# Kernel tuning notes

Measured on AMD Instinct MI355X. Metric: run time of the kernel, lower is better.

The kernel has to match this reference:

```python
import jax, jax.numpy as jnp
import numpy as np

L, D, H, IMG, P, B, E = 12, 768, 12, 224, 16, 32, 512
HD = D // H            # 64
FF = 4 * D             # 3072
SEQ = (IMG // P) ** 2 + 1  # 197


def _ln(x, w, b, eps=1e-5):
    m = x.mean(-1, keepdims=True)
    v = jnp.mean((x - m) ** 2, axis=-1, keepdims=True)
    return (x - m) * jax.lax.rsqrt(v + eps) * w + b


def setup_inputs() -> dict:
    key = jax.random.key(0)
    ks = jax.random.split(key, 10)
    r = lambda k, shape, s=0.02: (jax.random.normal(k, shape, jnp.float32) * s)
    return {
        'image': jax.random.normal(ks[0], (B, 3, IMG, IMG), jnp.float32),
        'conv_w': r(ks[1], (D, 3, P, P)),
        'cls_emb': r(ks[2], (D,)),
        'pos_emb': r(ks[3], (SEQ, D)),
        'ln_pre_w': jnp.ones((D,), jnp.float32), 'ln_pre_b': jnp.zeros((D,), jnp.float32),
        'ln1_w': jnp.ones((L, D), jnp.float32), 'ln1_b': jnp.zeros((L, D), jnp.float32),
        'qkv_w': r(ks[4], (L, 3 * D, D)), 'qkv_b': jnp.zeros((L, 3 * D), jnp.float32),
        'out_w': r(ks[5], (L, D, D)), 'out_b': jnp.zeros((L, D), jnp.float32),
        'ln2_w': jnp.ones((L, D), jnp.float32), 'ln2_b': jnp.zeros((L, D), jnp.float32),
        'fc_w': r(ks[6], (L, FF, D)), 'fc_b': jnp.zeros((L, FF), jnp.float32),
        'pr_w': r(ks[7], (L, D, FF)), 'pr_b': jnp.zeros((L, D), jnp.float32),
        'ln_post_w': jnp.ones((D,), jnp.float32), 'ln_post_b': jnp.zeros((D,), jnp.float32),
        'proj': r(ks[8], (D, E)),
    }


def reference(image, conv_w, cls_emb, pos_emb, ln_pre_w, ln_pre_b,
              ln1_w, ln1_b, qkv_w, qkv_b, out_w, out_b,
              ln2_w, ln2_b, fc_w, fc_b, pr_w, pr_b,
              ln_post_w, ln_post_b, proj):
    # patchify: conv stride=kernel=patch, no bias -> [B, D, 14, 14]
    x = jax.lax.conv_general_dilated(image, conv_w, (P, P), 'VALID',
                                     dimension_numbers=('NCHW', 'OIHW', 'NCHW'))
    x = x.reshape(B, D, -1).transpose(0, 2, 1)               # [B, 196, D]
    cls = jnp.broadcast_to(cls_emb, (B, 1, D))
    x = jnp.concatenate([cls, x], axis=1) + pos_emb          # [B, SEQ, D]
    x = _ln(x, ln_pre_w, ln_pre_b)
    x = x.transpose(1, 0, 2)                                  # [SEQ, B, D]
    scale = 1.0 / np.sqrt(HD).astype(np.float32)

    def step(x, p):
        l1w, l1b, qw, qb, ow, ob, l2w, l2b, fw, fb, pw, pb = p
        h = _ln(x, l1w, l1b)
        qkv = h @ qw.T + qb                                    # [SEQ, B, 3D]
        q, k, v = jnp.split(qkv, 3, axis=-1)
        heads = lambda t: t.reshape(SEQ, B * H, HD).transpose(1, 0, 2)  # [B*H, SEQ, HD]
        q = heads(q) * scale
        k = heads(k)
        v = heads(v)
        a = jax.nn.softmax(jnp.einsum('nsh,nth->nst', q, k), axis=-1)   # [B*H, SEQ, SEQ]
        o = jnp.einsum('nst,nth->nsh', a, v)                  # [B*H, SEQ, HD]
        o = o.transpose(1, 0, 2).reshape(SEQ, B, D)
        x = x + (o @ ow.T + ob)
        h = _ln(x, l2w, l2b)
        h = jax.nn.gelu(h @ fw.T + fb, approximate=False)      # torch nn.GELU (exact)
        x = x + (h @ pw.T + pb)
        return x, None

    x, _ = jax.lax.scan(step, x, (ln1_w, ln1_b, qkv_w, qkv_b, out_w, out_b,
                                  ln2_w, ln2_b, fc_w, fc_b, pr_w, pr_b))
    x = x.transpose(1, 0, 2)                                   # [B, SEQ, D]
    cls_tok = _ln(x[:, 0, :], ln_post_w, ln_post_b)
    feats = cls_tok @ proj                                     # [B, E]
    return feats / jnp.linalg.norm(feats, axis=-1, keepdims=True)
```

## Files before the change

### kernel.cpp

```cpp
#include <hip/hip_runtime.h>
#include <stdint.h>

#define SEQ 197
#define NB 32
#define NH 12
#define NTOK (SEQ*NB)
#define MPAD 6400
#define NPATCH 6272

typedef unsigned short u16;
typedef unsigned int u32;
typedef __attribute__((ext_vector_type(8))) short bv8;
typedef __attribute__((ext_vector_type(4))) float f32x4;

__device__ __forceinline__ u16 f2bf(float f){
  u32 u = __float_as_uint(f);
  u = (u + 0x7fffu + ((u >> 16) & 1u)) >> 16;
  return (u16)u;
}
__device__ __forceinline__ float bf2f(u16 h){ return __uint_as_float(((u32)h) << 16); }

#if defined(__has_builtin)
#if __has_builtin(__builtin_amdgcn_global_load_lds)
#define HAS_GLLDS 1
#endif
#endif

__device__ __forceinline__ void gl_lds16(const void* g, void* l){
#ifdef HAS_GLLDS
  __builtin_amdgcn_global_load_lds(
      (const __attribute__((address_space(1))) void*)(uintptr_t)g,
      (__attribute__((address_space(3))) void*)(u32)(uintptr_t)l, 16, 0, 0);
#else
  int lane = threadIdx.x & 63;
  uint4 v = *(const uint4*)((const char*)g);
  *(uint4*)((char*)l + lane*16) = v;
#endif
}

__device__ __forceinline__ void red2(float& a, float& b){
  #pragma unroll
  for (int o = 32; o > 0; o >>= 1){ a += __shfl_down(a, o); b += __shfl_down(b, o); }
  __shared__ float red[8];
  int w = threadIdx.x >> 6, ln = threadIdx.x & 63;
  if (ln == 0){ red[w] = a; red[4 + w] = b; }
  __syncthreads();
  a = red[0] + red[1] + red[2] + red[3];
  b = red[4] + red[5] + red[6] + red[7];
}

__global__ __launch_bounds__(256) void cvt_k(const float* __restrict__ src, u16* __restrict__ dst, int n4){
  int i = blockIdx.x * 256 + threadIdx.x;
  if (i >= n4) return;
  float4 f = ((const float4*)src)[i];
  u32 lo = (u32)f2bf(f.x) | ((u32)f2bf(f.y) << 16);
  u32 hi = (u32)f2bf(f.z) | ((u32)f2bf(f.w) << 16);
  ((uint2*)dst)[i] = make_uint2(lo, hi);
}

__global__ __launch_bounds__(256) void im2col_k(const float* __restrict__ img, u16* __restrict__ Ap){
  int gid = blockIdx.x * 256 + threadIdx.x;
  int row = gid / 768, k = gid - row * 768;
  int b = row / 196, p = row - b * 196;
  int pr = p / 14, pc = p - pr * 14;
  int c = k >> 8, r = k & 255;
  int ph = r >> 4, pw = r & 15;
  size_t src = ((size_t)(b * 3 + c) * 224 + (pr * 16 + ph)) * 224 + (pc * 16 + pw);
  Ap[gid] = f2bf(img[src]);
}

template<int EPI>
__global__ __launch_bounds__(256, 2)
void gemm_sw(const u16* __restrict__ A, const u16* __restrict__ Bw,
             const float* __restrict__ bias, float* __restrict__ Cf,
             u16* __restrict__ Cb, int N, int K, int Mreal,
             int RM, int RN, int tmT, int tnT)
{
  __shared__ __align__(16) u16 sA[128 * 64];
  __shared__ __align__(16) u16 sB[128 * 64];
  const int xcd = blockIdx.x & 7, pos = blockIdx.x >> 3;
  const int xm = xcd >> 1, xn = xcd & 1;
  const int tm = xm * RM + pos / RN;
  const int tn = xn * RN + pos % RN;
  if (tm >= tmT || tn >= tnT) return;

  const int tid = threadIdx.x;
  const int lane = tid & 63, wave = tid >> 6;
  const int wm = wave >> 1, wn = wave & 1;
  const int lr = lane & 15, g = lane >> 4, g4 = g * 4;
  const int KT = K >> 6;

  const int srow = lane >> 3;
  const int sch = (lane & 7) ^ srow;
  const u16* aB[4]; const u16* bB[4];
  u16* lA[4]; u16* lB[4];
  #pragma unroll
  for (int j = 0; j < 4; j++){
    int rr = wave * 32 + j * 8;
    aB[j] = A  + (size_t)(tm * 128 + rr + srow) * K + sch * 8;
    bB[j] = Bw + (size_t)(tn * 128 + rr + srow) * K + sch * 8;
    lA[j] = sA + rr * 64;
    lB[j] = sB + rr * 64;
  }

  f32x4 acc[4][4] = {};

  for (int kt = 0; kt < KT; ++kt){
    __syncthreads();
    #pragma unroll
    for (int j = 0; j < 4; j++) gl_lds16(aB[j] + (size_t)kt * 64, lA[j]);
    #pragma unroll
    for (int j = 0; j < 4; j++) gl_lds16(bB[j] + (size_t)kt * 64, lB[j]);
    __syncthreads();
    #pragma unroll
    for (int kk = 0; kk < 2; kk++){
      bv8 af[4], bf[4];
      #pragma unroll
      for (int mi = 0; mi < 4; mi++){
        int row = wm * 64 + mi * 16 + lr;
        af[mi] = *(const bv8*)((const char*)sA + row * 128 + ((kk * 64 + g * 16) ^ ((row & 7) << 4)));
      }
      #pragma unroll
      for (int ni = 0; ni < 4; ni++){
        int row = wn * 64 + ni * 16 + lr;
        bf[ni] = *(const bv8*)((const char*)sB + row * 128 + ((kk * 64 + g * 16) ^ ((row & 7) << 4)));
      }
      #pragma unroll
      for (int mi = 0; mi < 4; mi++)
        #pragma unroll
        for (int ni = 0; ni < 4; ni++)
          acc[mi][ni] = __builtin_amdgcn_mfma_f32_16x16x32_bf16(af[mi], bf[ni], acc[mi][ni], 0, 0, 0);
    }
  }

  if (EPI == 1 || EPI == 3){
    __syncthreads();
    u16* sC = sA;
    #pragma unroll
    for (int mi = 0; mi < 4; mi++){
      #pragma unroll
      for (int ni = 0; ni < 4; ni++){
        int bcol = wn * 64 + ni * 16 + lr;
        float bvs = bias[tn * 128 + bcol];
        #pragma unroll
        for (int j = 0; j < 4; j++){
          int brow = wm * 64 + mi * 16 + g4 + j;
          float v = acc[mi][ni][j] + bvs;
          if (EPI == 3) v = 0.5f * v * (1.f + erff(v * 0.70710678118654752f));
          *(u16*)((char*)sC + brow * 256 + ((bcol * 2) ^ ((brow & 7) << 4))) = f2bf(v);
        }
      }
    }
    __syncthreads();
    #pragma unroll
    for (int c = 0; c < 8; c++){
      int off = c * 4096 + tid * 16;
      int row = off >> 8;
      int colb = off & 255;
      uint4 v = *(const uint4*)((const char*)sC + row * 256 + (colb ^ ((row & 7) << 4)));
      *(uint4*)((char*)(Cb + (size_t)(tm * 128 + row) * N + tn * 128) + colb) = v;
    }
  } else {
    #pragma unroll
    for (int ni = 0; ni < 4; ni++){
      int col = tn * 128 + wn * 64 + ni * 16 + lr;
      float bvs = (EPI != 0) ? bias[col] : 0.f;
      #pragma unroll
      for (int mi = 0; mi < 4; mi++){
        int row0 = tm * 128 + wm * 64 + mi * 16 + g4;
        #pragma unroll
        for (int j = 0; j < 4; j++){
          int row = row0 + j;
          if (row < Mreal){
            float v = acc[mi][ni][j] + bvs;
            size_t idx = (size_t)row * N + col;
            if (EPI == 0) Cf[idx] = v;
            else          Cf[idx] += v;
          }
        }
      }
    }
  }
}

__global__ __launch_bounds__(256, 1) void attn_k(const u16* __restrict__ qkv, u16* __restrict__ o_out){
  __shared__ __align__(16) u16 sK[256 * 64];
  __shared__ __align__(16) u16 sVT[64 * 256];
  __shared__ __align__(16) u16 sP[4 * 64 * 64];
  const int bh = blockIdx.x;
  const int b = bh / NH, h = bh - b * NH;
  const int tid = threadIdx.x;
  const int lane = tid & 63, wave = tid >> 6;
  const int lr = lane & 15, g = lane >> 4;
  const int g4 = g * 4;
  const int wb = wave * 64;
  const u16* kbase = qkv + (size_t)b * SEQ * 2304 + h * 64 + 768;
  const u16* vbase = kbase + 768;

  bv8 qf[4][2];
  #pragma unroll
  for (int qt = 0; qt < 4; qt++){
    int q = wb + qt * 16 + lr; if (q > 196) q = 196;
    const u16* qr = qkv + (size_t)(b * SEQ + q) * 2304 + h * 64;
    #pragma unroll
    for (int kc = 0; kc < 2; kc++)
      qf[qt][kc] = *(const bv8*)(qr + kc * 32 + g * 8);
  }

  for (int i = tid; i < 197 * 32; i += 256){
    int r = i >> 5, c = i & 31;
    u32 kv_ = *(const u32*)(kbase + (size_t)r * 2304 + c * 2);
    *(u32*)((char*)sK + ((r * 128 + c * 4) ^ ((r & 7) << 4))) = kv_;
    u32 vv = *(const u32*)(vbase + (size_t)r * 2304 + c * 2);
    int hd0 = c * 2, hd1 = c * 2 + 1;
    *(u16*)((char*)sVT + ((hd0 * 512 + r * 2) ^ ((hd0 & 7) << 4))) = (u16)(vv & 0xffff);
    *(u16*)((char*)sVT + ((hd1 * 512 + r * 2) ^ ((hd1 & 7) << 4))) = (u16)(vv >> 16);
  }
  for (int i = tid; i < 59 * 32; i += 256){
    int r = 197 + (i >> 5), c = i & 31;
    *(u32*)((char*)sK + (r * 128 + c * 4)) = 0;
  }
  for (int i = tid; i < 59 * 64; i += 256){
    int kv = 197 + (i >> 6), hd = i & 63;
    *(u16*)((char*)sVT + ((hd * 512 + kv * 2) ^ ((hd & 7) << 4))) = 0;
  }
  __syncthreads();

  f32x4 acc_o[4][4] = {};
  float m_[4] = {-1e30f, -1e30f, -1e30f, -1e30f};
  float l_[4] = {0.f, 0.f, 0.f, 0.f};
  u16* sPw = sP + wave * 4096;

  for (int ch = 0; ch < 4; ++ch){
    f32x4 st[4][4] = {};
    #pragma unroll
    for (int kc = 0; kc < 2; kc++){
      bv8 kf[4];
      #pragma unroll
      for (int kvt = 0; kvt < 4; kvt++){
        int row = ch * 64 + kvt * 16 + lr;
        kf[kvt] = *(const bv8*)((const char*)sK + ((row * 128 + kc * 64 + g * 16) ^ ((row & 7) << 4)));
      }
      #pragma unroll
      for (int kvt = 0; kvt < 4; kvt++)
        #pragma unroll
        for (int qt = 0; qt < 4; qt++)
          st[kvt][qt] = __builtin_amdgcn_mfma_f32_16x16x32_bf16(kf[kvt], qf[qt][kc], st[kvt][qt], 0, 0, 0);
    }
    float fac[4];
    #pragma unroll
    for (int qt = 0; qt < 4; qt++){
      float mx = -1e30f;
      #pragma unroll
      for (int kvt = 0; kvt < 4; kvt++)
        #pragma unroll
        for (int j = 0; j < 4; j++){
          int kvg = ch * 64 + kvt * 16 + g4 + j;
          float s = st[kvt][qt][j] * 0.125f;
          s = (kvg < 197) ? s : -1e30f;
          st[kvt][qt][j] = s;
          mx = fmaxf(mx, s);
        }
      mx = fmaxf(mx, __shfl_xor(mx, 16));
      mx = fmaxf(mx, __shfl_xor(mx, 32));
      float nm = fmaxf(m_[qt], mx);
      fac[qt] = __expf(m_[qt] - nm);
      m_[qt] = nm;
      float ls = 0.f;
      #pragma unroll
      for (int kvt = 0; kvt < 4; kvt++)
        #pragma unroll
        for (int j = 0; j < 4; j++){
          float p = __expf(st[kvt][qt][j] - nm);
          st[kvt][qt][j] = p;
          ls += p;
        }
      ls += __shfl_xor(ls, 16);
      ls += __shfl_xor(ls, 32);
      l_[qt] = l_[qt] * fac[qt] + ls;
    }
    #pragma unroll
    for (int qt = 0; qt < 4; qt++)
      #pragma unroll
      for (int j = 0; j < 4; j++){
        float fj = __shfl(fac[qt], (lane & 48) | (g4 + j));
        #pragma unroll
        for (int nt = 0; nt < 4; nt++) acc_o[qt][nt][j] *= fj;
      }
    #pragma unroll
    for (int qt = 0; qt < 4; qt++){
      int row = qt * 16 + lr;
      #pragma unroll
      for (int kvt = 0; kvt < 4; kvt++){
        uint2 pk;
        pk.x = (u32)f2bf(st[kvt][qt][0]) | ((u32)f2bf(st[kvt][qt][1]) << 16);
        pk.y = (u32)f2bf(st[kvt][qt][2]) | ((u32)f2bf(st[kvt][qt][3]) << 16);
        *(uint2*)((char*)sPw + ((row * 128 + kvt * 32 + g * 8) ^ ((row & 7) << 4))) = pk;
      }
    }
    #pragma unroll
    for (int kc = 0; kc < 2; kc++){
      bv8 pa[4], vb[4];
      #pragma unroll
      for (int qt = 0; qt < 4; qt++){
        int row = qt * 16 + lr;
        pa[qt] = *(const bv8*)((const char*)sPw + ((row * 128 + kc * 64 + g * 16) ^ ((row & 7) << 4)));
      }
      #pragma unroll
      for (int nt = 0; nt < 4; nt++){
        int hd = nt * 16 + lr;
        vb[nt] = *(const bv8*)((const char*)sVT + ((hd * 512 + ch * 128 + kc * 64 + g * 16) ^ ((hd & 7) << 4)));
      }
      #pragma unroll
      for (int qt = 0; qt < 4; qt++)
        #pragma unroll
        for (int nt = 0; nt < 4; nt++)
          acc_o[qt][nt] = __builtin_amdgcn_mfma_f32_16x16x32_bf16(pa[qt], vb[nt], acc_o[qt][nt], 0, 0, 0);
    }
  }

  #pragma unroll
  for (int qt = 0; qt < 4; qt++)
    #pragma unroll
    for (int j = 0; j < 4; j++){
      float lj = __shfl(l_[qt], (lane & 48) | (g4 + j));
      float rl = 1.f / lj;
      int row = wb + qt * 16 + g4 + j;
      if (row < 197){
        u16* dst = o_out + (size_t)(b * SEQ + row) * 768 + h * 64;
        #pragma unroll
        for (int nt = 0; nt < 4; nt++)
          dst[nt * 16 + lr] = f2bf(acc_o[qt][nt][j] * rl);
      }
    }
}

__global__ __launch_bounds__(256) void embed_ln_k(const float* __restrict__ patch, const float* __restrict__ cls,
    const float* __restrict__ pos, const float* __restrict__ w, const float* __restrict__ bb, float* __restrict__ x)
{
  int t = blockIdx.x;
  int b = t / SEQ, s = t - b * SEQ;
  int tid = threadIdx.x;
  float v[3];
  #pragma unroll
  for (int i = 0; i < 3; i++){
    int d = tid + i * 256;
    float base = (s == 0) ? cls[d] : patch[(size_t)(b * 196 + s - 1) * 768 + d];
    v[i] = base + pos[s * 768 + d];
  }
  float sm = v[0] + v[1] + v[2];
  float sq = v[0]*v[0] + v[1]*v[1] + v[2]*v[2];
  red2(sm, sq);
  float m = sm * (1.f / 768.f);
  float rs = rsqrtf(sq * (1.f / 768.f) - m * m + 1e-5f);
  #pragma unroll
  for (int i = 0; i < 3; i++){
    int d = tid + i * 256;
    x[(size_t)t * 768 + d] = (v[i] - m) * rs * w[d] + bb[d];
  }
}

__global__ __launch_bounds__(256) void ln_bf16_k(const float* __restrict__ x, const float* __restrict__ w,
    const float* __restrict__ bb, u16* __restrict__ h)
{
  int t = blockIdx.x, tid = threadIdx.x;
  const float* xr = x + (size_t)t * 768;
  float v[3];
  #pragma unroll
  for (int i = 0; i < 3; i++) v[i] = xr[tid + i * 256];
  float sm = v[0] + v[1] + v[2];
  float sq = v[0]*v[0] + v[1]*v[1] + v[2]*v[2];
  red2(sm, sq);
  float m = sm * (1.f / 768.f);
  float rs = rsqrtf(sq * (1.f / 768.f) - m * m + 1e-5f);
  #pragma unroll
  for (int i = 0; i < 3; i++){
    int d = tid + i * 256;
    h[(size_t)t * 768 + d] = f2bf((v[i] - m) * rs * w[d] + bb[d]);
  }
}

__global__ __launch_bounds__(256) void ln_cls_k(const float* __restrict__ x, const float* __restrict__ w,
    const float* __restrict__ bb, float* __restrict__ cls)
{
  int b = blockIdx.x, tid = threadIdx.x;
  const float* xr = x + (size_t)b * SEQ * 768;
  float v[3];
  #pragma unroll
  for (int i = 0; i < 3; i++) v[i] = xr[tid + i * 256];
  float sm = v[0] + v[1] + v[2];
  float sq = v[0]*v[0] + v[1]*v[1] + v[2]*v[2];
  red2(sm, sq);
  float m = sm * (1.f / 768.f);
  float rs = rsqrtf(sq * (1.f / 768.f) - m * m + 1e-5f);
  #pragma unroll
  for (int i = 0; i < 3; i++){
    int d = tid + i * 256;
    cls[b * 768 + d] = (v[i] - m) * rs * w[d] + bb[d];
  }
}

__global__ __launch_bounds__(256) void proj_k(const float* __restrict__ cls, const float* __restrict__ P,
                                              float* __restrict__ feats){
  int gid = blockIdx.x * 256 + threadIdx.x;
  int b = gid >> 9, e = gid & 511;
  const float* c = cls + b * 768;
  float a0 = 0, a1 = 0, a2 = 0, a3 = 0;
  for (int d = 0; d < 768; d += 4){
    a0 += c[d]     * P[(size_t)d * 512 + e];
    a1 += c[d + 1] * P[(size_t)(d + 1) * 512 + e];
    a2 += c[d + 2] * P[(size_t)(d + 2) * 512 + e];
    a3 += c[d + 3] * P[(size_t)(d + 3) * 512 + e];
  }
  feats[gid] = (a0 + a1) + (a2 + a3);
}

__global__ __launch_bounds__(256) void norm_k(const float* __restrict__ feats, float* __restrict__ out){
  int b = blockIdx.x, tid = threadIdx.x;
  float v0 = feats[b * 512 + tid], v1 = feats[b * 512 + 256 + tid];
  float sq = v0 * v0 + v1 * v1, dummy = 0.f;
  red2(sq, dummy);
  float inv = 1.f / sqrtf(sq);
  out[b * 512 + tid] = v0 * inv;
  out[b * 512 + 256 + tid] = v1 * inv;
}

extern "C" void kernel_launch(void* const* d_in, const int* in_sizes, int n_in,
                              void* d_out, int out_size, void* d_ws, size_t ws_size,
                              hipStream_t stream)
{
  const float* image   = (const float*)d_in[0];
  const float* conv_w  = (const float*)d_in[1];
  const float* cls_emb = (const float*)d_in[2];
  const float* pos_emb = (const float*)d_in[3];
  const float* lnprew  = (const float*)d_in[4];
  const float* lnpreb  = (const float*)d_in[5];
  const float* ln1w    = (const float*)d_in[6];
  const float* ln1b    = (const float*)d_in[7];
  const float* qkvw    = (const float*)d_in[8];
  const float* qkvb    = (const float*)d_in[9];
  const float* outw    = (const float*)d_in[10];
  const float* outb    = (const float*)d_in[11];
  const float* ln2w    = (const float*)d_in[12];
  const float* ln2b    = (const float*)d_in[13];
  const float* fcw     = (const float*)d_in[14];
  const float* fcb     = (const float*)d_in[15];
  const float* prw     = (const float*)d_in[16];
  const float* prb     = (const float*)d_in[17];
  const float* lnpostw = (const float*)d_in[18];
  const float* lnpostb = (const float*)d_in[19];
  const float* proj    = (const float*)d_in[20];
  (void)in_sizes; (void)n_in; (void)out_size;

  const size_t QW = (size_t)2304 * 768, OW = (size_t)768 * 768;
  const size_t FW = (size_t)3072 * 768, PW = (size_t)768 * 3072;
  const size_t CW = (size_t)768 * 768;

  char* p = (char*)d_ws;
  auto alloc = [&](size_t bytes)->char*{ char* r = p; p += (bytes + 255) & ~(size_t)255; return r; };
  float* x     = (float*)alloc((size_t)MPAD * 768 * 4);
  u16*   h     = (u16*)  alloc((size_t)MPAD * 768 * 2);
  u16*   qkvB  = (u16*)  alloc((size_t)MPAD * 2304 * 2);
  u16*   attno = (u16*)  alloc((size_t)MPAD * 768 * 2);
  u16*   ffh   = (u16*)  alloc((size_t)MPAD * 3072 * 2);
  u16*   Ap    = (u16*)  alloc((size_t)NPATCH * 768 * 2);
  float* patch = (float*)alloc((size_t)NPATCH * 768 * 4);
  float* clsb  = (float*)alloc((size_t)32 * 768 * 4);
  float* feats = (float*)alloc((size_t)32 * 512 * 4);
  u16*   cwb   = (u16*)  alloc(CW * 2);
  size_t base_used = (size_t)(p - (char*)d_ws);
  size_t full_need = (QW + OW + FW + PW) * 12 * 2;
  bool full = (base_used + full_need + 4096 <= ws_size);

  u16 *wq = nullptr, *wo = nullptr, *wf = nullptr, *wp = nullptr;
  u16 *sq_ = nullptr, *so_ = nullptr, *sf_ = nullptr, *sp_ = nullptr;
  if (full){
    wq = (u16*)alloc(QW * 12 * 2); wo = (u16*)alloc(OW * 12 * 2);
    wf = (u16*)alloc(FW * 12 * 2); wp = (u16*)alloc(PW * 12 * 2);
  } else {
    sq_ = (u16*)alloc(QW * 2); so_ = (u16*)alloc(OW * 2);
    sf_ = (u16*)alloc(FW * 2); sp_ = (u16*)alloc(PW * 2);
  }
  if ((size_t)(p - (char*)d_ws) > ws_size) return;

  { int n4 = (int)(CW / 4); cvt_k<<<(n4 + 255) / 256, 256, 0, stream>>>(conv_w, cwb, n4); }
  if (full){
    int n4;
    n4 = (int)(QW * 12 / 4); cvt_k<<<(n4 + 255) / 256, 256, 0, stream>>>(qkvw, wq, n4);
    n4 = (int)(OW * 12 / 4); cvt_k<<<(n4 + 255) / 256, 256, 0, stream>>>(outw, wo, n4);
    n4 = (int)(FW * 12 / 4); cvt_k<<<(n4 + 255) / 256, 256, 0, stream>>>(fcw,  wf, n4);
    n4 = (int)(PW * 12 / 4); cvt_k<<<(n4 + 255) / 256, 256, 0, stream>>>(prw,  wp, n4);
  }

  im2col_k<<<(NPATCH * 768) / 256, 256, 0, stream>>>(image, Ap);
  gemm_sw<0><<<8 * 13 * 3, 256, 0, stream>>>(Ap, cwb, nullptr, patch, nullptr, 768, 768, NPATCH, 13, 3, 49, 6);
  embed_ln_k<<<NTOK, 256, 0, stream>>>(patch, cls_emb, pos_emb, lnprew, lnpreb, x);

  for (int l = 0; l < 12; l++){
    const u16 *WQ, *WO, *WF, *WP;
    if (full){
      WQ = wq + (size_t)l * QW; WO = wo + (size_t)l * OW;
      WF = wf + (size_t)l * FW; WP = wp + (size_t)l * PW;
    } else {
      int n4;
      n4 = (int)(QW / 4); cvt_k<<<(n4 + 255) / 256, 256, 0, stream>>>(qkvw + (size_t)l * QW, sq_, n4);
      n4 = (int)(OW / 4); cvt_k<<<(n4 + 255) / 256, 256, 0, stream>>>(outw + (size_t)l * OW, so_, n4);
      n4 = (int)(FW / 4); cvt_k<<<(n4 + 255) / 256, 256, 0, stream>>>(fcw  + (size_t)l * FW, sf_, n4);
      n4 = (int)(PW / 4); cvt_k<<<(n4 + 255) / 256, 256, 0, stream>>>(prw  + (size_t)l * PW, sp_, n4);
      WQ = sq_; WO = so_; WF = sf_; WP = sp_;
    }
    ln_bf16_k<<<NTOK, 256, 0, stream>>>(x, ln1w + l * 768, ln1b + l * 768, h);
    gemm_sw<1><<<8 * 13 * 9, 256, 0, stream>>>(h, WQ, qkvb + l * 2304, nullptr, qkvB, 2304, 768, NTOK, 13, 9, 50, 18);
    attn_k<<<NB * NH, 256, 0, stream>>>(qkvB, attno);
    gemm_sw<2><<<8 * 13 * 3, 256, 0, stream>>>(attno, WO, outb + l * 768, x, nullptr, 768, 768, NTOK, 13, 3, 50, 6);
    ln_bf16_k<<<NTOK, 256, 0, stream>>>(x, ln2w + l * 768, ln2b + l * 768, h);
    gemm_sw<3><<<8 * 13 * 12, 256, 0, stream>>>(h, WF, fcb + l * 3072, nullptr, ffh, 3072, 768, NTOK, 13, 12, 50, 24);
    gemm_sw<2><<<8 * 13 * 3, 256, 0, stream>>>(ffh, WP, prb + l * 768, x, nullptr, 768, 3072, NTOK, 13, 3, 50, 6);
  }

  ln_cls_k<<<NB, 256, 0, stream>>>(x, lnpostw, lnpostb, clsb);
  proj_k<<<(NB * 512) / 256, 256, 0, stream>>>(clsb, proj, feats);
  norm_k<<<NB, 256, 0, stream>>>(feats, (float*)d_out);
}
```

Baseline: 3.130 ms.

## Double-buffer GEMM LDS tiles with async prefetch overlapping MFMA compute

Replaces the single-buffered GEMM main loop with a two-stage LDS ping-pong. The next K tile is issued via global_load_lds while MFMAs run on the current one, using explicit vmcnt/lgkmcnt waits, raw barriers and s_setprio around the MFMA block. The goal is to hide global-memory latency that the old load, sync, compute sequence exposed. It doubles LDS use to 64KB per block, which may cut occupancy from two blocks per CU, and the hand-written waitcnt logic depends on an exact count of outstanding loads.

```diff
diff --git a/kernel.cpp b/kernel.cpp
--- a/kernel.cpp
+++ b/kernel.cpp
@@ -71,13 +71,15 @@
 
 template<int EPI>
 __global__ __launch_bounds__(256, 2)
-void gemm_sw(const u16* __restrict__ A, const u16* __restrict__ Bw,
-             const float* __restrict__ bias, float* __restrict__ Cf,
-             u16* __restrict__ Cb, int N, int K, int Mreal,
-             int RM, int RN, int tmT, int tnT)
+void gemm_2ph(const u16* __restrict__ A, const u16* __restrict__ Bw,
+              const float* __restrict__ bias, float* __restrict__ Cf,
+              u16* __restrict__ Cb, int N, int K, int Mreal,
+              int RM, int RN, int tmT, int tnT)
 {
-  __shared__ __align__(16) u16 sA[128 * 64];
-  __shared__ __align__(16) u16 sB[128 * 64];
+  __shared__ __align__(16) u16 sA0[128 * 64];
+  __shared__ __align__(16) u16 sB0[128 * 64];
+  __shared__ __align__(16) u16 sA1[128 * 64];
+  __shared__ __align__(16) u16 sB1[128 * 64];
   const int xcd = blockIdx.x & 7, pos = blockIdx.x >> 3;
   const int xm = xcd >> 1, xn = xcd & 1;
   const int tm = xm * RM + pos / RN;
@@ -93,49 +95,68 @@
   const int srow = lane >> 3;
   const int sch = (lane & 7) ^ srow;
   const u16* aB[4]; const u16* bB[4];
-  u16* lA[4]; u16* lB[4];
   #pragma unroll
   for (int j = 0; j < 4; j++){
     int rr = wave * 32 + j * 8;
     aB[j] = A  + (size_t)(tm * 128 + rr + srow) * K + sch * 8;
     bB[j] = Bw + (size_t)(tn * 128 + rr + srow) * K + sch * 8;
-    lA[j] = sA + rr * 64;
-    lB[j] = sB + rr * 64;
   }
 
   f32x4 acc[4][4] = {};
 
-  for (int kt = 0; kt < KT; ++kt){
-    __syncthreads();
-    #pragma unroll
-    for (int j = 0; j < 4; j++) gl_lds16(aB[j] + (size_t)kt * 64, lA[j]);
-    #pragma unroll
-    for (int j = 0; j < 4; j++) gl_lds16(bB[j] + (size_t)kt * 64, lB[j]);
-    __syncthreads();
-    #pragma unroll
-    for (int kk = 0; kk < 2; kk++){
-      bv8 af[4], bf[4];
-      #pragma unroll
-      for (int mi = 0; mi < 4; mi++){
-        int row = wm * 64 + mi * 16 + lr;
-        af[mi] = *(const bv8*)((const char*)sA + row * 128 + ((kk * 64 + g * 16) ^ ((row & 7) << 4)));
-      }
-      #pragma unroll
-      for (int ni = 0; ni < 4; ni++){
-        int row = wn * 64 + ni * 16 + lr;
-        bf[ni] = *(const bv8*)((const char*)sB + row * 128 + ((kk * 64 + g * 16) ^ ((row & 7) << 4)));
-      }
+  auto stage = [&](int kt, u16* dA, u16* dB){
+    #pragma unroll
+    for (int j = 0; j < 4; j++)
+      gl_lds16(aB[j] + (size_t)kt * 64, dA + (wave * 32 + j * 8) * 64);
+    #pragma unroll
+    for (int j = 0; j < 4; j++)
+      gl_lds16(bB[j] + (size_t)kt * 64, dB + (wave * 32 + j * 8) * 64);
+  };
+  auto tile = [&](const u16* sA, const u16* sB, u16* dA, u16* dB, int ktNext, bool doStage, bool last){
+    if (last) asm volatile("s_waitcnt vmcnt(0)" ::: "memory");
+    else      asm volatile("s_waitcnt vmcnt(8)" ::: "memory");
+    __builtin_amdgcn_s_barrier();
+    bv8 af[4][2], bf[4][2];
+    #pragma unroll
+    for (int mi = 0; mi < 4; mi++){
+      int row = wm * 64 + mi * 16 + lr;
+      #pragma unroll
+      for (int kk = 0; kk < 2; kk++)
+        af[mi][kk] = *(const bv8*)((const char*)sA + row * 128 + ((kk * 64 + g * 16) ^ ((row & 7) << 4)));
+    }
+    #pragma unroll
+    for (int ni = 0; ni < 4; ni++){
+      int row = wn * 64 + ni * 16 + lr;
+      #pragma unroll
+      for (int kk = 0; kk < 2; kk++)
+        bf[ni][kk] = *(const bv8*)((const char*)sB + row * 128 + ((kk * 64 + g * 16) ^ ((row & 7) << 4)));
+    }
+    asm volatile("s_waitcnt lgkmcnt(0)" ::: "memory");
+    __builtin_amdgcn_s_barrier();
+    if (doStage) stage(ktNext, dA, dB);
+    __builtin_amdgcn_s_setprio(1);
+    #pragma unroll
+    for (int kk = 0; kk < 2; kk++)
       #pragma unroll
       for (int mi = 0; mi < 4; mi++)
         #pragma unroll
         for (int ni = 0; ni < 4; ni++)
-          acc[mi][ni] = __builtin_amdgcn_mfma_f32_16x16x32_bf16(af[mi], bf[ni], acc[mi][ni], 0, 0, 0);
-    }
-  }
+          acc[mi][ni] = __builtin_amdgcn_mfma_f32_16x16x32_bf16(af[mi][kk], bf[ni][kk], acc[mi][ni], 0, 0, 0);
+    __builtin_amdgcn_s_setprio(0);
+  };
+
+  stage(0, sA0, sB0);
+  stage(1, sA1, sB1);
+  int t = 0;
+  for (; t + 2 < KT; t += 2){
+    tile(sA0, sB0, sA0, sB0, t + 2, true,  false);
+    tile(sA1, sB1, sA1, sB1, t + 3, true,  false);
+  }
+  tile(sA0, sB0, sA0, sB0, 0, false, false);
+  tile(sA1, sB1, sA1, sB1, 0, false, true);
 
   if (EPI == 1 || EPI == 3){
     __syncthreads();
-    u16* sC = sA;
     #pragma unroll
     for (int mi = 0; mi < 4; mi++){
       #pragma unroll
@@ -147,7 +168,8 @@
           int brow = wm * 64 + mi * 16 + g4 + j;
           float v = acc[mi][ni][j] + bvs;
           if (EPI == 3) v = 0.5f * v * (1.f + erff(v * 0.70710678118654752f));
-          *(u16*)((char*)sC + brow * 256 + ((bcol * 2) ^ ((brow & 7) << 4))) = f2bf(v);
+          char* base = (char*)(brow < 64 ? sA0 : sB0);
+          *(u16*)(base + (brow & 63) * 256 + ((bcol * 2) ^ ((brow & 7) << 4))) = f2bf(v);
         }
       }
     }
@@ -157,7 +179,8 @@
       int off = c * 4096 + tid * 16;
       int row = off >> 8;
       int colb = off & 255;
-      uint4 v = *(const uint4*)((const char*)sC + row * 256 + (colb ^ ((row & 7) << 4)));
+      const char* base = (const char*)(row < 64 ? sA0 : sB0);
+      uint4 v = *(const uint4*)(base + (row & 63) * 256 + (colb ^ ((row & 7) << 4)));
       *(uint4*)((char*)(Cb + (size_t)(tm * 128 + row) * N + tn * 128) + colb) = v;
     }
   } else {
@@ -493,7 +516,7 @@
   }
 
   im2col_k<<<(NPATCH * 768) / 256, 256, 0, stream>>>(image, Ap);
-  gemm_sw<0><<<8 * 13 * 3, 256, 0, stream>>>(Ap, cwb, nullptr, patch, nullptr, 768, 768, NPATCH, 13, 3, 49, 6);
+  gemm_2ph<0><<<8 * 13 * 3, 256, 0, stream>>>(Ap, cwb, nullptr, patch, nullptr, 768, 768, NPATCH, 13, 3, 49, 6);
   embed_ln_k<<<NTOK, 256, 0, stream>>>(patch, cls_emb, pos_emb, lnprew, lnpreb, x);
 
   for (int l = 0; l < 12; l++){
@@ -510,12 +533,12 @@
       WQ = sq_; WO = so_; WF = sf_; WP = sp_;
     }
     ln_bf16_k<<<NTOK, 256, 0, stream>>>(x, ln1w + l * 768, ln1b + l * 768, h);
-    gemm_sw<1><<<8 * 13 * 9, 256, 0, stream>>>(h, WQ, qkvb + l * 2304, nullptr, qkvB, 2304, 768, NTOK, 13, 9, 50, 18);
+    gemm_2ph<1><<<8 * 13 * 9, 256, 0, stream>>>(h, WQ, qkvb + l * 2304, nullptr, qkvB, 2304, 768, NTOK, 13, 9, 50, 18);
     attn_k<<<NB * NH, 256, 0, stream>>>(qkvB, attno);
-    gemm_sw<2><<<8 * 13 * 3, 256, 0, stream>>>(attno, WO, outb + l * 768, x, nullptr, 768, 768, NTOK, 13, 3, 50, 6);
+    gemm_2ph<2><<<8 * 13 * 3, 256, 0, stream>>>(attno, WO, outb + l * 768, x, nullptr, 768, 768, NTOK, 13, 3, 50, 6);
     ln_bf16_k<<<NTOK, 256, 0, stream>>>(x, ln2w + l * 768, ln2b + l * 768, h);
-    gemm_sw<3><<<8 * 13 * 12, 256, 0, stream>>>(h, WF, fcb + l * 3072, nullptr, ffh, 3072, 768, NTOK, 13, 12, 50, 24);
-    gemm_sw<2><<<8 * 13 * 3, 256, 0, stream>>>(ffh, WP, prb + l * 768, x, nullptr, 768, 3072, NTOK, 13, 3, 50, 6);
+    gemm_2ph<3><<<8 * 13 * 12, 256, 0, stream>>>(h, WF, fcb + l * 3072, nullptr, ffh, 3072, 768, NTOK, 13, 12, 50, 24);
+    gemm_2ph<2><<<8 * 13 * 3, 256, 0, stream>>>(ffh, WP, prb + l * 768, x, nullptr, 768, 3072, NTOK, 13, 3, 50, 6);
   }
 
   ln_cls_k<<<NB, 256, 0, stream>>>(x, lnpostw, lnpostb, clsb);
```

Result: faster. 2.911 ms (-7.0%).
